# Kernel tuning notes

Measured on AMD Instinct MI355X. Metric: run time of the kernel, lower is better.

## Reference

```python
import jax, jax.numpy as jnp
import numpy as np

FSIZE = 128   # fsize
ANUM = 16     # number of agents
CNUM = 2048   # number of cities
BATCH = 64


def setup_inputs() -> dict:
    key = jax.random.key(0)
    ks = jax.random.split(key, 6)
    f = FSIZE
    N = CNUM + 2 * ANUM
    s = 0.02
    return {
        "nfeature": jax.random.normal(ks[0], (BATCH, f, N), jnp.float32),
        # torch Linear weights are [out, in]
        "Wg": jax.random.normal(ks[1], (f, 4 * f), jnp.float32) * s,   # glb_embedding
        "bg": jnp.zeros((f,), jnp.float32),
        "Wc": jax.random.normal(ks[2], (3 * f, 2 * f), jnp.float32) * s,  # city_embedding
        "bc": jnp.zeros((3 * f,), jnp.float32),
        "Wa": jax.random.normal(ks[3], (f, 3 * f), jnp.float32) * s,   # agent_embedding
        "ba": jnp.zeros((f,), jnp.float32),
        "Wp": jax.random.normal(ks[4], (f, f), jnp.float32) * s,       # project_out
        "bp": jnp.zeros((f,), jnp.float32),
        "step": 1,
        "anum": ANUM,
    }


def reference(nfeature, Wg, bg, Wc, bc, Wa, ba, Wp, bp, step, anum):
    nf = jnp.transpose(nfeature, (0, 2, 1))  # [B, N, f]
    B, N, f = nf.shape
    cnum = N - 2 * anum
    city = nf[:, :cnum]                       # [B, cnum, f]
    a_start = nf[:, cnum:cnum + anum]         # [B, anum, f]
    a_end = nf[:, cnum + anum:]               # [B, anum, f]

    # global context via max pooling over segments -> glb_embedding
    glb = jnp.concatenate([nf.max(1), city.max(1), a_start.max(1), a_end.max(1)], axis=1)  # [B, 4f]
    deglb = (glb @ Wg.T + bg)[:, None, :]     # [B, 1, f]

    # mean-pooled global context -> same glb_embedding -> free agent token
    ave = jnp.concatenate([nf.mean(1), city.mean(1), a_start.mean(1), a_end.mean(1)], axis=1)
    free_agent = (ave @ Wg.T + bg)[:, None, :]  # [B, 1, f]

    # city keys/values/logit-keys: x, y, z
    city_feat = jnp.concatenate([jnp.broadcast_to(deglb, (B, cnum, f)), city], axis=2)  # [B, cnum, 2f]
    xyz = city_feat @ Wc.T + bc               # [B, cnum, 3f]
    x, y, z = jnp.split(xyz, 3, axis=2)       # each [B, cnum, f]

    # agent queries
    agent_feat = jnp.concatenate(
        [jnp.broadcast_to(deglb, (B, anum, f)), a_start, a_end], axis=2)  # [B, anum, 3f]
    af = agent_feat @ Wa.T + ba               # [B, anum, f]
    if step > 0:
        af = jnp.concatenate([af, free_agent], axis=1)  # [B, anum+1, f]

    scale = 1.0 / jnp.sqrt(jnp.float32(f))
    ucj = jnp.einsum('baf,bcf->bac', af, x) * scale           # [B, A, cnum]
    new_af = jnp.einsum('bac,bcf->baf', jax.nn.softmax(ucj, axis=2), y)
    new_af = new_af @ Wp.T + bp                                # project_out
    logits = jnp.tanh(jnp.einsum('baf,bcf->bac', new_af, z) * scale) * 10.0  # [B, A, cnum]
    probs = jax.nn.softmax(jnp.transpose(logits, (0, 2, 1)), axis=2)         # [B, cnum, A]
    return probs
```

## Files before the change

kernel.cpp:

```cpp
#include <hip/hip_runtime.h>
#include <math.h>

#define F 128
#define NTOT 2080
#define CN 2048
#define AN 16
#define NA 17

__device__ __forceinline__ float wmax(float v){
  #pragma unroll
  for(int m=32;m;m>>=1) v = fmaxf(v, __shfl_xor(v, m, 64));
  return v;
}
__device__ __forceinline__ float wsum(float v){
  #pragma unroll
  for(int m=32;m;m>>=1) v += __shfl_xor(v, m, 64);
  return v;
}

__global__ __launch_bounds__(256) void k0t_transpose(
      const float* __restrict__ Wg, const float* __restrict__ Wc,
      const float* __restrict__ Wp, const float* __restrict__ Wa,
      float* __restrict__ WgT, float* __restrict__ WcT,
      float* __restrict__ WpT, float* __restrict__ WaT){
  __shared__ float tile[32][33];
  const int z = blockIdx.z;
  const float* src; float* dst; int R, C;
  if(z==0){ src=Wg; dst=WgT; R=128; C=512; }
  else if(z==1){ src=Wc; dst=WcT; R=384; C=256; }
  else if(z==2){ src=Wp; dst=WpT; R=128; C=128; }
  else { src=Wa; dst=WaT; R=128; C=384; }
  const int c0 = blockIdx.x*32, r0 = blockIdx.y*32;
  if(c0>=C || r0>=R) return;
  const int tx = threadIdx.x&31, ty = threadIdx.x>>5;
  #pragma unroll
  for(int rr=0;rr<4;rr++)
    tile[ty+rr*8][tx] = src[(size_t)(r0+ty+rr*8)*C + c0 + tx];
  __syncthreads();
  #pragma unroll
  for(int rr=0;rr<4;rr++)
    dst[(size_t)(c0+ty+rr*8)*R + r0 + tx] = tile[tx][ty+rr*8];
}

__global__ __launch_bounds__(128) void k0a_wpy(const float* __restrict__ Wp, const float* __restrict__ Wc,
                                               float* __restrict__ Wpy){
  const int k = blockIdx.x, i = threadIdx.x;
  float acc = 0.f;
  const float* wp = Wp + (size_t)k*F;
  for(int j=0;j<F;j++) acc += wp[j]*Wc[(size_t)(128+j)*256 + 128 + i];
  Wpy[k*F+i] = acc;
}

__global__ __launch_bounds__(128) void k0b_m1(const float* __restrict__ Wc, const float* __restrict__ Wpy,
                                              float* __restrict__ M1){
  const int jc = blockIdx.x, i = threadIdx.x;
  float acc = 0.f;
  for(int k=0;k<F;k++) acc += Wc[(size_t)(256+k)*256 + 128 + jc]*Wpy[k*F+i];
  M1[jc*F+i] = acc;
}

__global__ __launch_bounds__(256) void k1_reduce(const float* __restrict__ nf,
                                                 float* __restrict__ glb, float* __restrict__ ave){
  const int j = blockIdx.x, b = blockIdx.y, tid = threadIdx.x;
  const float4* row = (const float4*)(nf + (size_t)(b*F + j)*NTOT);
  float cmax=-INFINITY, csum=0.f, smax=-INFINITY, ssum=0.f, emax=-INFINITY, esum=0.f;
  for(int n4 = tid; n4 < 520; n4 += 256){
    float4 v = row[n4];
    float mx = fmaxf(fmaxf(v.x,v.y), fmaxf(v.z,v.w));
    float sm = (v.x+v.y)+(v.z+v.w);
    if(n4 < 512){ cmax=fmaxf(cmax,mx); csum+=sm; }
    else if(n4 < 516){ smax=fmaxf(smax,mx); ssum+=sm; }
    else { emax=fmaxf(emax,mx); esum+=sm; }
  }
  __shared__ float red[4][6];
  cmax=wmax(cmax); csum=wsum(csum); smax=wmax(smax); ssum=wsum(ssum); emax=wmax(emax); esum=wsum(esum);
  const int lane = tid&63, wid = tid>>6;
  if(lane==0){ red[wid][0]=cmax; red[wid][1]=csum; red[wid][2]=smax; red[wid][3]=ssum; red[wid][4]=emax; red[wid][5]=esum; }
  __syncthreads();
  if(tid==0){
    float cM=red[0][0], cS=red[0][1], sM=red[0][2], sS=red[0][3], eM=red[0][4], eS=red[0][5];
    for(int w=1;w<4;w++){ cM=fmaxf(cM,red[w][0]); cS+=red[w][1]; sM=fmaxf(sM,red[w][2]); sS+=red[w][3]; eM=fmaxf(eM,red[w][4]); eS+=red[w][5]; }
    const int gb = b*4*F;
    glb[gb + j]       = fmaxf(cM, fmaxf(sM,eM));
    glb[gb + F + j]   = cM;
    glb[gb + 2*F + j] = sM;
    glb[gb + 3*F + j] = eM;
    float tS = cS+sS+eS;
    ave[gb + j]       = tS / 2080.f;
    ave[gb + F + j]   = cS / 2048.f;
    ave[gb + 2*F + j] = sS / 16.f;
    ave[gb + 3*F + j] = eS / 16.f;
  }
}

__global__ __launch_bounds__(256) void k2a_prep(
    const float* __restrict__ WgT, const float* __restrict__ bg,
    const float* __restrict__ WcT, const float* __restrict__ Wc, const float* __restrict__ bc,
    const float* __restrict__ WpT, const float* __restrict__ bp,
    const float* __restrict__ Wpy,
    const float* __restrict__ glb, const float* __restrict__ ave,
    float* __restrict__ deglb_g, float* __restrict__ fa_g, float* __restrict__ cx,
    float* __restrict__ czc, float* __restrict__ vz, float* __restrict__ szc){
  const int b = blockIdx.x, tid = threadIdx.x;
  __shared__ float glb_s[512], ave_s[512];
  __shared__ float deglb_s[F], cvec_s[3*F], cpy_s[F];
  for(int i=tid;i<512;i+=256){ glb_s[i]=glb[b*512+i]; ave_s[i]=ave[b*512+i]; }
  __syncthreads();
  {
    const int j = tid&127;
    const float* src = (tid<128)? glb_s : ave_s;
    float a0=0.f,a1=0.f,a2=0.f,a3=0.f;
    for(int k=0;k<512;k+=4){
      a0 += WgT[(size_t)(k+0)*128+j]*src[k+0];
      a1 += WgT[(size_t)(k+1)*128+j]*src[k+1];
      a2 += WgT[(size_t)(k+2)*128+j]*src[k+2];
      a3 += WgT[(size_t)(k+3)*128+j]*src[k+3];
    }
    float d = (a0+a1)+(a2+a3) + bg[j];
    if(tid<128){ deglb_s[j]=d; deglb_g[b*F+j]=d; }
    else fa_g[b*F+j]=d;
  }
  __syncthreads();
  for(int i=tid;i<3*F;i+=256){
    float a0=0.f,a1=0.f,a2=0.f,a3=0.f;
    for(int k=0;k<F;k+=4){
      a0 += WcT[(size_t)(k+0)*384+i]*deglb_s[k+0];
      a1 += WcT[(size_t)(k+1)*384+i]*deglb_s[k+1];
      a2 += WcT[(size_t)(k+2)*384+i]*deglb_s[k+2];
      a3 += WcT[(size_t)(k+3)*384+i]*deglb_s[k+3];
    }
    float v = (a0+a1)+(a2+a3) + bc[i];
    cvec_s[i]=v;
    if(i<F) cx[b*F+i]=v;
  }
  __syncthreads();
  if(tid<128){
    const int j = tid;
    float a0=0.f,a1=0.f,a2=0.f,a3=0.f;
    for(int k=0;k<F;k+=4){
      a0 += WpT[(size_t)(k+0)*128+j]*cvec_s[128+k+0];
      a1 += WpT[(size_t)(k+1)*128+j]*cvec_s[128+k+1];
      a2 += WpT[(size_t)(k+2)*128+j]*cvec_s[128+k+2];
      a3 += WpT[(size_t)(k+3)*128+j]*cvec_s[128+k+3];
    }
    cpy_s[j] = (a0+a1)+(a2+a3) + bp[j];
  } else {
    const int j = tid-128;
    float a0=0.f,a1=0.f,a2=0.f,a3=0.f;
    for(int k=0;k<F;k+=4){
      a0 += Wpy[(size_t)(k+0)*128+j]*cvec_s[256+k+0];
      a1 += Wpy[(size_t)(k+1)*128+j]*cvec_s[256+k+1];
      a2 += Wpy[(size_t)(k+2)*128+j]*cvec_s[256+k+2];
      a3 += Wpy[(size_t)(k+3)*128+j]*cvec_s[256+k+3];
    }
    vz[b*F+j] = (a0+a1)+(a2+a3);
  }
  __syncthreads();
  if(tid<128){
    const int j = tid;
    float a0=0.f,a1=0.f,a2=0.f,a3=0.f;
    for(int k=0;k<F;k+=4){
      a0 += Wc[(size_t)(256+k+0)*256 + 128 + j]*cpy_s[k+0];
      a1 += Wc[(size_t)(256+k+1)*256 + 128 + j]*cpy_s[k+1];
      a2 += Wc[(size_t)(256+k+2)*256 + 128 + j]*cpy_s[k+2];
      a3 += Wc[(size_t)(256+k+3)*256 + 128 + j]*cpy_s[k+3];
    }
    czc[b*F+j] = (a0+a1)+(a2+a3);
  } else if(tid<192){
    const int lane = tid-128;
    float p = cpy_s[lane]*cvec_s[256+lane] + cpy_s[64+lane]*cvec_s[256+64+lane];
    p = wsum(p);
    if(lane==0) szc[b]=p;
  }
}

__global__ __launch_bounds__(256) void k2c_agents(
    const float* __restrict__ nf, const float* __restrict__ WaT, const float* __restrict__ ba,
    const float* __restrict__ Wc,
    const float* __restrict__ deglb_g, const float* __restrict__ fa_g, const float* __restrict__ cx,
    float* __restrict__ afx, float* __restrict__ sx){
  const int a = blockIdx.x, b = blockIdx.y, tid = threadIdx.x;
  __shared__ float src_s[384];
  __shared__ float af_s[F], cx_s[F];
  if(tid<128){ src_s[tid] = deglb_g[b*F+tid]; cx_s[tid]=cx[b*F+tid]; }
  else if(a<16){
    const int j = tid-128;
    src_s[128+j] = nf[(size_t)(b*F+j)*NTOT + CN + a];
    src_s[256+j] = nf[(size_t)(b*F+j)*NTOT + CN + AN + a];
  }
  __syncthreads();
  if(a<16){
    if(tid<128){
      const int j = tid;
      float a0=0.f,a1=0.f,a2=0.f,a3=0.f;
      for(int k=0;k<384;k+=4){
        a0 += WaT[(size_t)(k+0)*128+j]*src_s[k+0];
        a1 += WaT[(size_t)(k+1)*128+j]*src_s[k+1];
        a2 += WaT[(size_t)(k+2)*128+j]*src_s[k+2];
        a3 += WaT[(size_t)(k+3)*128+j]*src_s[k+3];
      }
      af_s[j] = (a0+a1)+(a2+a3) + ba[j];
    }
  } else if(tid<128){
    af_s[tid] = fa_g[b*F+tid];
  }
  __syncthreads();
  if(tid<128){
    const int j = tid;
    float a0=0.f,a1=0.f,a2=0.f,a3=0.f;
    for(int i=0;i<F;i+=4){
      a0 += af_s[i+0]*Wc[(size_t)(i+0)*256 + 128 + j];
      a1 += af_s[i+1]*Wc[(size_t)(i+1)*256 + 128 + j];
      a2 += af_s[i+2]*Wc[(size_t)(i+2)*256 + 128 + j];
      a3 += af_s[i+3]*Wc[(size_t)(i+3)*256 + 128 + j];
    }
    afx[((size_t)b*NA+a)*F + j] = (a0+a1)+(a2+a3);
  } else if(tid<192){
    const int lane = tid-128;
    float p = af_s[lane]*cx_s[lane] + af_s[64+lane]*cx_s[64+lane];
    p = wsum(p);
    if(lane==0) sx[b*NA+a]=p;
  }
}

__global__ __launch_bounds__(256) void k3_scores(const float* __restrict__ nf, const float* __restrict__ afx,
      const float* __restrict__ sx, float* __restrict__ ucj, float* __restrict__ pmax){
  const int b = blockIdx.y, tid = threadIdx.x;
  const int c = blockIdx.x*256 + tid;
  __shared__ float afx_s[NA*F]; __shared__ float sx_s[NA];
  for(int o=tid;o<NA*F;o+=256) afx_s[o]=afx[(size_t)b*NA*F+o];
  if(tid<NA) sx_s[tid]=sx[b*NA+tid];
  __syncthreads();
  float acc[NA];
  #pragma unroll
  for(int a=0;a<NA;a++) acc[a]=0.f;
  const float* base = nf + (size_t)b*F*NTOT + c;
  #pragma unroll 4
  for(int i=0;i<F;i++){
    float v = base[(size_t)i*NTOT];
    #pragma unroll
    for(int a=0;a<NA;a++) acc[a] += afx_s[a*F+i]*v;
  }
  const float scale = 0.088388347648318447f;
  float uc[NA];
  #pragma unroll
  for(int a=0;a<NA;a++){
    uc[a] = (acc[a]+sx_s[a])*scale;
    ucj[((size_t)b*NA + a)*CN + c] = uc[a];
  }
  __shared__ float red[4][NA];
  const int lane = tid&63, wid = tid>>6;
  #pragma unroll
  for(int a=0;a<NA;a++){
    float m = wmax(uc[a]);
    if(lane==0) red[wid][a]=m;
  }
  __syncthreads();
  if(tid<NA){
    float m = fmaxf(fmaxf(red[0][tid],red[1][tid]), fmaxf(red[2][tid],red[3][tid]));
    pmax[(b*NA+tid)*8 + blockIdx.x] = m;
  }
}

__global__ __launch_bounds__(256) void k4_softmax(float* __restrict__ ucj, const float* __restrict__ pmax,
        float* __restrict__ rowsum){
  const int a = blockIdx.x, b = blockIdx.y, tid = threadIdx.x;
  float m=-INFINITY;
  #pragma unroll
  for(int k=0;k<8;k++) m = fmaxf(m, pmax[(b*NA+a)*8+k]);
  float* row = ucj + ((size_t)b*NA+a)*CN;
  float s=0.f;
  for(int c=tid;c<CN;c+=256){ float e = __expf(row[c]-m); row[c]=e; s+=e; }
  s = wsum(s);
  __shared__ float red[4];
  const int lane=tid&63, wid=tid>>6;
  if(lane==0) red[wid]=s;
  __syncthreads();
  if(tid==0) rowsum[b*NA+a]=red[0]+red[1]+red[2]+red[3];
}

__global__ __launch_bounds__(256) void k5_taccum(const float* __restrict__ nf,
      const float* __restrict__ attn, float* __restrict__ tpart){
  const int b = blockIdx.y, tid = threadIdx.x;
  const int c0 = blockIdx.x*256;
  __shared__ float4 nf4_s[F*16];
  __shared__ float4 at4_s[NA*16];
  const int i = tid&127, h = tid>>7;
  const int A0 = h*8;
  float acc[9];
  #pragma unroll
  for(int a=0;a<9;a++) acc[a]=0.f;
  for(int s4=0;s4<4;s4++){
    const int cs = c0 + s4*64;
    __syncthreads();
    for(int idx=tid; idx<F*16; idx+=256){
      const int ii=idx>>4, g=idx&15;
      nf4_s[ii*16 + (g^(ii&15))] = *(const float4*)(nf + (size_t)(b*F+ii)*NTOT + cs + g*4);
    }
    for(int idx=tid; idx<NA*16; idx+=256){
      const int a=idx>>4, g=idx&15;
      at4_s[idx] = *(const float4*)(attn + ((size_t)b*NA+a)*CN + cs + g*4);
    }
    __syncthreads();
    #pragma unroll 2
    for(int g=0; g<16; g++){
      float4 v = nf4_s[i*16 + (g^(i&15))];
      #pragma unroll
      for(int a=0;a<9;a++){
        float4 w = at4_s[(A0+a)*16+g];
        acc[a] += w.x*v.x + w.y*v.y + w.z*v.z + w.w*v.w;
      }
    }
  }
  float* dst = tpart + (size_t)blockIdx.x*64*NA*F + (size_t)b*NA*F;
  #pragma unroll
  for(int a=0;a<9;a++){
    if(h==0 || a>0) dst[(A0+a)*F + i] = acc[a];
  }
}

__global__ __launch_bounds__(128) void k5b_final(const float* __restrict__ M1,
      const float* __restrict__ tpart, const float* __restrict__ rowsum,
      const float* __restrict__ czc, const float* __restrict__ vz, const float* __restrict__ szc,
      float* __restrict__ afz, float* __restrict__ szv){
  const int a = blockIdx.x, b = blockIdx.y, tid = threadIdx.x;
  __shared__ float tn_s[F];
  float s = 0.f;
  #pragma unroll
  for(int k=0;k<8;k++) s += tpart[(size_t)k*64*NA*F + ((size_t)b*NA+a)*F + tid];
  tn_s[tid] = s / rowsum[b*NA+a];
  __syncthreads();
  float acc = 0.f;
  const float* m = M1 + (size_t)tid*F;
  for(int i=0;i<F;i++) acc += m[i]*tn_s[i];
  afz[((size_t)b*NA+a)*F + tid] = acc + czc[b*F+tid];
  float p = tn_s[tid]*vz[b*F+tid];
  p = wsum(p);
  __shared__ float red[2];
  if((tid&63)==0) red[tid>>6]=p;
  __syncthreads();
  if(tid==0) szv[b*NA+a] = red[0]+red[1] + szc[b];
}

__global__ __launch_bounds__(256) void k6_out(const float* __restrict__ nf, const float* __restrict__ afz,
      const float* __restrict__ szv, const int* __restrict__ step, float* __restrict__ out){
  const int b = blockIdx.y, tid = threadIdx.x;
  const int c = blockIdx.x*256 + tid;
  __shared__ float afz_s[NA*F]; __shared__ float sz_s[NA];
  for(int o=tid;o<NA*F;o+=256) afz_s[o]=afz[(size_t)b*NA*F+o];
  if(tid<NA) sz_s[tid]=szv[b*NA+tid];
  __syncthreads();
  const int A = (step[0] > 0) ? NA : AN;
  float acc[NA];
  #pragma unroll
  for(int a=0;a<NA;a++) acc[a]=0.f;
  const float* base = nf + (size_t)b*F*NTOT + c;
  #pragma unroll 4
  for(int i=0;i<F;i++){
    float v = base[(size_t)i*NTOT];
    #pragma unroll
    for(int a=0;a<NA;a++) acc[a] += afz_s[a*F+i]*v;
  }
  const float scale = 0.088388347648318447f;
  float l[NA];
  #pragma unroll
  for(int a=0;a<NA;a++) l[a] = tanhf((acc[a]+sz_s[a])*scale)*10.f;
  const bool f17 = (A==NA);
  float m = l[0];
  #pragma unroll
  for(int a=1;a<AN;a++) m = fmaxf(m,l[a]);
  if(f17) m = fmaxf(m,l[16]);
  float ssum=0.f;
  #pragma unroll
  for(int a=0;a<AN;a++){ float e=__expf(l[a]-m); l[a]=e; ssum+=e; }
  float e16=__expf(l[16]-m);
  if(f17){ ssum+=e16; }
  const float inv = 1.f/ssum;
  float* op = out + (size_t)(b*CN + c)*A;
  #pragma unroll
  for(int a=0;a<AN;a++) op[a]=l[a]*inv;
  if(f17) op[16]=e16*inv;
}

extern "C" void kernel_launch(void* const* d_in, const int* in_sizes, int n_in,
                              void* d_out, int out_size, void* d_ws, size_t ws_size,
                              hipStream_t stream){
  const float* nf = (const float*)d_in[0];
  const float* Wg = (const float*)d_in[1];
  const float* bg = (const float*)d_in[2];
  const float* Wc = (const float*)d_in[3];
  const float* bc = (const float*)d_in[4];
  const float* Wa = (const float*)d_in[5];
  const float* ba = (const float*)d_in[6];
  const float* Wp = (const float*)d_in[7];
  const float* bp = (const float*)d_in[8];
  const int*  step = (const int*)d_in[9];
  float* out = (float*)d_out;

  float* ws = (float*)d_ws;
  float* glb     = ws;
  float* ave     = glb + 64*512;
  float* afx     = ave + 64*512;
  float* sx      = afx + 64*NA*F;
  float* Wpy     = sx + 64*NA;
  float* M1      = Wpy + F*F;
  float* czc     = M1 + F*F;
  float* vz      = czc + 64*F;
  float* szc     = vz + 64*F;
  float* rowsum  = szc + 64;
  float* deglb_g = rowsum + 64*NA;
  float* fa_g    = deglb_g + 64*F;
  float* cx      = fa_g + 64*F;
  float* WgT     = cx + 64*F;
  float* WcT     = WgT + 512*F;
  float* WpT     = WcT + 256*384;
  float* WaT     = WpT + F*F;
  float* tpart   = WaT + 384*F;
  float* afz     = tpart + 8*64*NA*F;
  float* szv     = afz + 64*NA*F;
  float* ucj     = szv + 64*NA;
  float* pmax    = ucj + (size_t)64*NA*CN;

  k0t_transpose<<<dim3(16,12,4),256,0,stream>>>(Wg,Wc,Wp,Wa, WgT,WcT,WpT,WaT);
  k0a_wpy<<<F,F,0,stream>>>(Wp, Wc, Wpy);
  k0b_m1<<<F,F,0,stream>>>(Wc, Wpy, M1);
  k1_reduce<<<dim3(128,64),256,0,stream>>>(nf, glb, ave);
  k2a_prep<<<64,256,0,stream>>>(WgT,bg, WcT,Wc,bc, WpT,bp, Wpy, glb,ave, deglb_g,fa_g,cx, czc,vz,szc);
  k2c_agents<<<dim3(NA,64),256,0,stream>>>(nf, WaT,ba,Wc, deglb_g,fa_g,cx, afx,sx);
  k3_scores<<<dim3(8,64),256,0,stream>>>(nf, afx, sx, ucj, pmax);
  k4_softmax<<<dim3(NA,64),256,0,stream>>>(ucj, pmax, rowsum);
  k5_taccum<<<dim3(8,64),256,0,stream>>>(nf, ucj, tpart);
  k5b_final<<<dim3(NA,64),128,0,stream>>>(M1, tpart, rowsum, czc, vz, szc, afz, szv);
  k6_out<<<dim3(8,64),256,0,stream>>>(nf, afz, szv, step, out);
}
```

Before: 166.7 us.

## Fuse scores, softmax and attention accumulation into one flash-style kernel

Merges the score, softmax and weighted-accumulation kernels into a single kernel per 256-city chunk. Exponentials are kept in shared memory under a chunk-local max, and per-chunk max and sum are stored. The final kernel rescales the partial accumulations with an online-softmax correction. This drops the global ucj score buffer round trips and two launches, at the cost of more shared memory per block (about 57KB), which may lower occupancy.

```diff
diff --git a/kernel.cpp b/kernel.cpp
--- a/kernel.cpp
+++ b/kernel.cpp
@@ -223,73 +223,62 @@
   }
 }
 
-__global__ __launch_bounds__(256) void k3_scores(const float* __restrict__ nf, const float* __restrict__ afx,
-      const float* __restrict__ sx, float* __restrict__ ucj, float* __restrict__ pmax){
+__global__ __launch_bounds__(256) void k35_flash(const float* __restrict__ nf,
+      const float* __restrict__ afx, const float* __restrict__ sx,
+      float* __restrict__ pmax, float* __restrict__ psum, float* __restrict__ tpart){
   const int b = blockIdx.y, tid = threadIdx.x;
-  const int c = blockIdx.x*256 + tid;
-  __shared__ float afx_s[NA*F]; __shared__ float sx_s[NA];
+  const int chunk = blockIdx.x, c0 = chunk*256;
+  __shared__ float afx_s[NA*F];
+  __shared__ float sx_s[NA];
+  __shared__ float at_s[NA*256];
+  __shared__ float4 nf4_s[F*16];
+  __shared__ float red_s[4][NA];
+  __shared__ float m_s[NA];
   for(int o=tid;o<NA*F;o+=256) afx_s[o]=afx[(size_t)b*NA*F+o];
   if(tid<NA) sx_s[tid]=sx[b*NA+tid];
   __syncthreads();
   float acc[NA];
   #pragma unroll
   for(int a=0;a<NA;a++) acc[a]=0.f;
-  const float* base = nf + (size_t)b*F*NTOT + c;
-  #pragma unroll 4
-  for(int i=0;i<F;i++){
-    float v = base[(size_t)i*NTOT];
-    #pragma unroll
-    for(int a=0;a<NA;a++) acc[a] += afx_s[a*F+i]*v;
+  {
+    const float* base = nf + (size_t)b*F*NTOT + c0 + tid;
+    #pragma unroll 4
+    for(int i=0;i<F;i++){
+      float v = base[(size_t)i*NTOT];
+      #pragma unroll
+      for(int a=0;a<NA;a++) acc[a] += afx_s[a*F+i]*v;
+    }
   }
   const float scale = 0.088388347648318447f;
-  float uc[NA];
+  #pragma unroll
+  for(int a=0;a<NA;a++) acc[a] = (acc[a]+sx_s[a])*scale;
+  const int lane = tid&63, wid = tid>>6;
   #pragma unroll
   for(int a=0;a<NA;a++){
-    uc[a] = (acc[a]+sx_s[a])*scale;
-    ucj[((size_t)b*NA + a)*CN + c] = uc[a];
-  }
-  __shared__ float red[4][NA];
-  const int lane = tid&63, wid = tid>>6;
+    float m = wmax(acc[a]);
+    if(lane==0) red_s[wid][a]=m;
+  }
+  __syncthreads();
+  if(tid<NA){
+    float m = fmaxf(fmaxf(red_s[0][tid],red_s[1][tid]), fmaxf(red_s[2][tid],red_s[3][tid]));
+    m_s[tid]=m;
+    pmax[(b*NA+tid)*8 + chunk]=m;
+  }
+  __syncthreads();
   #pragma unroll
   for(int a=0;a<NA;a++){
-    float m = wmax(uc[a]);
-    if(lane==0) red[wid][a]=m;
-  }
-  __syncthreads();
-  if(tid<NA){
-    float m = fmaxf(fmaxf(red[0][tid],red[1][tid]), fmaxf(red[2][tid],red[3][tid]));
-    pmax[(b*NA+tid)*8 + blockIdx.x] = m;
-  }
-}
-
-__global__ __launch_bounds__(256) void k4_softmax(float* __restrict__ ucj, const float* __restrict__ pmax,
-        float* __restrict__ rowsum){
-  const int a = blockIdx.x, b = blockIdx.y, tid = threadIdx.x;
-  float m=-INFINITY;
-  #pragma unroll
-  for(int k=0;k<8;k++) m = fmaxf(m, pmax[(b*NA+a)*8+k]);
-  float* row = ucj + ((size_t)b*NA+a)*CN;
-  float s=0.f;
-  for(int c=tid;c<CN;c+=256){ float e = __expf(row[c]-m); row[c]=e; s+=e; }
-  s = wsum(s);
-  __shared__ float red[4];
-  const int lane=tid&63, wid=tid>>6;
-  if(lane==0) red[wid]=s;
-  __syncthreads();
-  if(tid==0) rowsum[b*NA+a]=red[0]+red[1]+red[2]+red[3];
-}
-
-__global__ __launch_bounds__(256) void k5_taccum(const float* __restrict__ nf,
-      const float* __restrict__ attn, float* __restrict__ tpart){
-  const int b = blockIdx.y, tid = threadIdx.x;
-  const int c0 = blockIdx.x*256;
-  __shared__ float4 nf4_s[F*16];
-  __shared__ float4 at4_s[NA*16];
-  const int i = tid&127, h = tid>>7;
-  const int A0 = h*8;
-  float acc[9];
-  #pragma unroll
-  for(int a=0;a<9;a++) acc[a]=0.f;
+    float e = __expf(acc[a]-m_s[a]);
+    at_s[a*256+tid]=e;
+    float s = wsum(e);
+    if(lane==0) red_s[wid][a]=s;
+  }
+  __syncthreads();
+  if(tid<NA)
+    psum[(b*NA+tid)*8 + chunk] = red_s[0][tid]+red_s[1][tid]+red_s[2][tid]+red_s[3][tid];
+  const int i = tid&127, h = tid>>7, A0 = h*8;
+  float ta[9];
+  #pragma unroll
+  for(int a=0;a<9;a++) ta[a]=0.f;
   for(int s4=0;s4<4;s4++){
     const int cs = c0 + s4*64;
     __syncthreads();
@@ -297,38 +286,42 @@
       const int ii=idx>>4, g=idx&15;
       nf4_s[ii*16 + (g^(ii&15))] = *(const float4*)(nf + (size_t)(b*F+ii)*NTOT + cs + g*4);
     }
-    for(int idx=tid; idx<NA*16; idx+=256){
-      const int a=idx>>4, g=idx&15;
-      at4_s[idx] = *(const float4*)(attn + ((size_t)b*NA+a)*CN + cs + g*4);
-    }
     __syncthreads();
     #pragma unroll 2
     for(int g=0; g<16; g++){
       float4 v = nf4_s[i*16 + (g^(i&15))];
       #pragma unroll
       for(int a=0;a<9;a++){
-        float4 w = at4_s[(A0+a)*16+g];
-        acc[a] += w.x*v.x + w.y*v.y + w.z*v.z + w.w*v.w;
+        float4 w = *(const float4*)&at_s[(A0+a)*256 + s4*64 + g*4];
+        ta[a] += w.x*v.x + w.y*v.y + w.z*v.z + w.w*v.w;
       }
     }
   }
-  float* dst = tpart + (size_t)blockIdx.x*64*NA*F + (size_t)b*NA*F;
+  float* dst = tpart + (size_t)chunk*64*NA*F + (size_t)b*NA*F;
   #pragma unroll
   for(int a=0;a<9;a++){
-    if(h==0 || a>0) dst[(A0+a)*F + i] = acc[a];
-  }
-}
-
-__global__ __launch_bounds__(128) void k5b_final(const float* __restrict__ M1,
-      const float* __restrict__ tpart, const float* __restrict__ rowsum,
+    if(h==0 || a>0) dst[(A0+a)*F + i] = ta[a];
+  }
+}
+
+__global__ __launch_bounds__(128) void k5c_final(const float* __restrict__ M1,
+      const float* __restrict__ tpart, const float* __restrict__ pmax, const float* __restrict__ psum,
       const float* __restrict__ czc, const float* __restrict__ vz, const float* __restrict__ szc,
       float* __restrict__ afz, float* __restrict__ szv){
   const int a = blockIdx.x, b = blockIdx.y, tid = threadIdx.x;
   __shared__ float tn_s[F];
+  const float* pm = pmax + (b*NA+a)*8;
+  const float* ps = psum + (b*NA+a)*8;
+  float M=-INFINITY;
+  #pragma unroll
+  for(int k=0;k<8;k++) M = fmaxf(M, pm[k]);
+  float w[8]; float rs=0.f;
+  #pragma unroll
+  for(int k=0;k<8;k++){ w[k]=__expf(pm[k]-M); rs += ps[k]*w[k]; }
   float s = 0.f;
   #pragma unroll
-  for(int k=0;k<8;k++) s += tpart[(size_t)k*64*NA*F + ((size_t)b*NA+a)*F + tid];
-  tn_s[tid] = s / rowsum[b*NA+a];
+  for(int k=0;k<8;k++) s += tpart[(size_t)k*64*NA*F + ((size_t)b*NA+a)*F + tid]*w[k];
+  tn_s[tid] = s / rs;
   __syncthreads();
   float acc = 0.f;
   const float* m = M1 + (size_t)tid*F;
@@ -407,8 +400,9 @@
   float* czc     = M1 + F*F;
   float* vz      = czc + 64*F;
   float* szc     = vz + 64*F;
-  float* rowsum  = szc + 64;
-  float* deglb_g = rowsum + 64*NA;
+  float* pmax    = szc + 64;
+  float* psum    = pmax + 64*NA*8;
+  float* deglb_g = psum + 64*NA*8;
   float* fa_g    = deglb_g + 64*F;
   float* cx      = fa_g + 64*F;
   float* WgT     = cx + 64*F;
@@ -418,8 +412,6 @@
   float* tpart   = WaT + 384*F;
   float* afz     = tpart + 8*64*NA*F;
   float* szv     = afz + 64*NA*F;
-  float* ucj     = szv + 64*NA;
-  float* pmax    = ucj + (size_t)64*NA*CN;
 
   k0t_transpose<<<dim3(16,12,4),256,0,stream>>>(Wg,Wc,Wp,Wa, WgT,WcT,WpT,WaT);
   k0a_wpy<<<F,F,0,stream>>>(Wp, Wc, Wpy);
@@ -427,9 +419,7 @@
   k1_reduce<<<dim3(128,64),256,0,stream>>>(nf, glb, ave);
   k2a_prep<<<64,256,0,stream>>>(WgT,bg, WcT,Wc,bc, WpT,bp, Wpy, glb,ave, deglb_g,fa_g,cx, czc,vz,szc);
   k2c_agents<<<dim3(NA,64),256,0,stream>>>(nf, WaT,ba,Wc, deglb_g,fa_g,cx, afx,sx);
-  k3_scores<<<dim3(8,64),256,0,stream>>>(nf, afx, sx, ucj, pmax);
-  k4_softmax<<<dim3(NA,64),256,0,stream>>>(ucj, pmax, rowsum);
-  k5_taccum<<<dim3(8,64),256,0,stream>>>(nf, ucj, tpart);
-  k5b_final<<<dim3(NA,64),128,0,stream>>>(M1, tpart, rowsum, czc, vz, szc, afz, szv);
+  k35_flash<<<dim3(8,64),256,0,stream>>>(nf, afx, sx, pmax, psum, tpart);
+  k5c_final<<<dim3(NA,64),128,0,stream>>>(M1, tpart, pmax, psum, czc, vz, szc, afz, szv);
   k6_out<<<dim3(8,64),256,0,stream>>>(nf, afz, szv, step, out);
 }
```

After: 158.0 us. 5.3% less time.
